# Kernel optimization log

Measured on AMD Instinct MI355X. Metric: run time of the kernel, lower is better.

The kernel has to match this reference:

```python
import jax, jax.numpy as jnp
import numpy as np

TEMPERATURE = 0.07
EPS = 1e-12  # matches F.normalize eps

def _l2norm(x, axis):
    n = jnp.sqrt(jnp.sum(x * x, axis=axis, keepdims=True))
    return x / jnp.maximum(n, EPS)

def setup_inputs() -> dict:
    key = jax.random.key(0)
    features = jax.random.normal(key, (512, 256), dtype=jnp.float32)
    return {"features": features}

def reference(features) -> jnp.ndarray:
    B = features.shape[0]
    f = _l2norm(features, axis=1)                      # [B, D]
    fi = f[:, None, :]                                 # broadcast over j
    fj = f[None, :, :]                                 # broadcast over i
    mutual = fi * fj                                   # [B, B, D]
    gate_i = fi * mutual
    gate_j = fj * mutual
    # torch broadcasting: + features adds f[j, k] along trailing dims
    feats_self_i = _l2norm(fi * gate_i + f, axis=2)
    feats_other_i = _l2norm(fi * gate_j + f, axis=2)
    feats_other_j = _l2norm(fj * gate_i + f, axis=2)
    # note: features_self_j is computed in the original but never used in any dot product

    raw_self_i = jnp.einsum('ik,ijk->ij', f, feats_self_i) / TEMPERATURE
    raw_self_j = jnp.einsum('ik,ijk->ij', f, feats_other_j) / TEMPERATURE  # (original uses other_j here)
    raw_other_i = jnp.einsum('ik,ijk->ij', f, feats_other_i) / TEMPERATURE
    raw_other_j = jnp.einsum('ik,ijk->ij', f, feats_other_j) / TEMPERATURE

    logits_mask = 1.0 - jnp.eye(B, dtype=f.dtype)      # zero out diagonal
    exp_sum = (jnp.exp(raw_self_i) + jnp.exp(raw_self_j)
               + jnp.exp(raw_other_i) + jnp.exp(raw_other_j)) * logits_mask
    vs_all = jnp.sum(exp_sum, axis=1, keepdims=True)   # [B, 1]

    log_prob = raw_self_i - jnp.log(vs_all)            # [B, B]
    mean_log_prob_pos = jnp.sum(log_prob, axis=1) / B
    loss = -jnp.mean(mean_log_prob_pos)
    return loss
```

## Files before the change

### kernel.cpp

```cpp
#include <hip/hip_runtime.h>
#include <math.h>

#define Bq 512
#define Dq 256

__device__ __forceinline__ float waveReduceSum(float v) {
    #pragma unroll
    for (int off = 32; off > 0; off >>= 1)
        v += __shfl_xor(v, off, 64);
    return v;
}

__global__ __launch_bounds__(256) void prep_kernel(
        const float* __restrict__ feat,
        float* __restrict__ fT, float* __restrict__ C1, float* __restrict__ C2,
        float* __restrict__ A1, float* __restrict__ A2) {
    int i = blockIdx.x;
    int k = threadIdx.x;
    float x = feat[i * Dq + k];
    float ss = waveReduceSum(x * x);
    __shared__ float wsum[4];
    int wid = threadIdx.x >> 6, lane = threadIdx.x & 63;
    if (lane == 0) wsum[wid] = ss;
    __syncthreads();
    float tot = wsum[0] + wsum[1] + wsum[2] + wsum[3];
    float n = fmaxf(sqrtf(tot), 1e-12f);
    float a = x / n;
    float a2 = a * a;
    float a3 = a2 * a;
    float c0 = 1.0f + a3;
    fT[k * Bq + i] = a;
    A1[i * Dq + k] = a;
    A2[i * Dq + k] = a2;
    C1[i * Dq + k] = a * c0;
    C2[i * Dq + k] = c0 * c0;
}

__global__ __launch_bounds__(512) void pair_kernel(
        const float* __restrict__ fT,
        const float* __restrict__ C1, const float* __restrict__ C2,
        const float* __restrict__ A1, const float* __restrict__ A2,
        float* __restrict__ Sv, float* __restrict__ Vv) {
    const int i = blockIdx.x;
    const int t = threadIdx.x;

    __shared__ __align__(16) float s_c1[Dq];
    __shared__ __align__(16) float s_c2[Dq];
    __shared__ __align__(16) float s_a1[Dq];
    __shared__ __align__(16) float s_a2[Dq];
    if (t < Dq) {
        s_c1[t] = C1[i * Dq + t];
        s_c2[t] = C2[i * Dq + t];
        s_a1[t] = A1[i * Dq + t];
        s_a2[t] = A2[i * Dq + t];
    }
    __syncthreads();

    float du = 0.f, nu = 0.f, dv = 0.f, nv = 0.f;
    const float* __restrict__ bp = fT + t;

    #pragma unroll 2
    for (int k0 = 0; k0 < Dq; k0 += 8) {
        float b[8];
        #pragma unroll
        for (int u = 0; u < 8; ++u) b[u] = bp[(k0 + u) * Bq];

        float4 q1a = *(const float4*)(s_c1 + k0), q1b = *(const float4*)(s_c1 + k0 + 4);
        float4 q2a = *(const float4*)(s_c2 + k0), q2b = *(const float4*)(s_c2 + k0 + 4);
        float4 q3a = *(const float4*)(s_a1 + k0), q3b = *(const float4*)(s_a1 + k0 + 4);
        float4 q4a = *(const float4*)(s_a2 + k0), q4b = *(const float4*)(s_a2 + k0 + 4);
        const float c1[8] = {q1a.x, q1a.y, q1a.z, q1a.w, q1b.x, q1b.y, q1b.z, q1b.w};
        const float c2[8] = {q2a.x, q2a.y, q2a.z, q2a.w, q2b.x, q2b.y, q2b.z, q2b.w};
        const float a1[8] = {q3a.x, q3a.y, q3a.z, q3a.w, q3b.x, q3b.y, q3b.z, q3b.w};
        const float a2[8] = {q4a.x, q4a.y, q4a.z, q4a.w, q4b.x, q4b.y, q4b.z, q4b.w};

        #pragma unroll
        for (int u = 0; u < 8; ++u) {
            float b1 = b[u];
            float bb = b1 * b1;
            float w  = fmaf(a2[u], b1, 1.0f);
            float wb = w * b1;
            du = fmaf(c1[u], b1, du);
            nu = fmaf(c2[u], bb, nu);
            dv = fmaf(a1[u], wb, dv);
            nv = fmaf(wb,    wb, nv);
        }
    }

    const float Tinv = 1.0f / 0.07f;
    float raw_s = du / fmaxf(sqrtf(nu), 1e-12f) * Tinv;
    float raw_o = dv / fmaxf(sqrtf(nv), 1e-12f) * Tinv;

    float sS = raw_s;
    float sV = (t == i) ? 0.f : (expf(raw_s) + 3.0f * expf(raw_o));

    sS = waveReduceSum(sS);
    sV = waveReduceSum(sV);
    __shared__ float redS[8], redV[8];
    int wid = t >> 6, lane = t & 63;
    if (lane == 0) { redS[wid] = sS; redV[wid] = sV; }
    __syncthreads();
    if (t == 0) {
        float S = 0.f, V = 0.f;
        #pragma unroll
        for (int w2 = 0; w2 < 8; ++w2) { S += redS[w2]; V += redV[w2]; }
        Sv[i] = S;
        Vv[i] = V;
    }
}

__global__ __launch_bounds__(512) void final_kernel(
        const float* __restrict__ Sv, const float* __restrict__ Vv,
        float* __restrict__ out) {
    int i = threadIdx.x;
    float t = Sv[i] * (1.0f / Bq) - logf(Vv[i]);
    t = waveReduceSum(t);
    __shared__ float red[8];
    int wid = i >> 6, lane = i & 63;
    if (lane == 0) red[wid] = t;
    __syncthreads();
    if (i == 0) {
        float s = 0.f;
        #pragma unroll
        for (int w = 0; w < 8; ++w) s += red[w];
        out[0] = -s / (float)Bq;
    }
}

extern "C" void kernel_launch(void* const* d_in, const int* in_sizes, int n_in,
                              void* d_out, int out_size, void* d_ws, size_t ws_size,
                              hipStream_t stream) {
    const float* feat = (const float*)d_in[0];
    float* ws = (float*)d_ws;
    float* fT = ws;
    float* C1 = fT + Bq * Dq;
    float* C2 = C1 + Bq * Dq;
    float* A1 = C2 + Bq * Dq;
    float* A2 = A1 + Bq * Dq;
    float* Sv = A2 + Bq * Dq;
    float* Vv = Sv + Bq;

    prep_kernel<<<Bq, Dq, 0, stream>>>(feat, fT, C1, C2, A1, A2);
    pair_kernel<<<Bq, 512, 0, stream>>>(fT, C1, C2, A1, A2, Sv, Vv);
    final_kernel<<<1, Bq, 0, stream>>>(Sv, Vv, (float*)d_out);
}
```

Measured before the change: 76.86 us.

## Compute per-row coefficients in pair kernel and fuse final reduction via last-block atomic

The prep kernel now writes only the transposed normalized features and per-row norms instead of four extra coefficient arrays. The pair kernel recomputes the coefficients from the raw features into shared memory. The separate final reduction kernel is removed: each block publishes its row term, and the last block to increment an atomic counter sums them. This cuts global writes and one kernel launch, at the cost of an atomic counter and a release/acquire handshake between blocks.

```diff
diff --git a/kernel.cpp b/kernel.cpp
--- a/kernel.cpp
+++ b/kernel.cpp
@@ -13,8 +13,8 @@
 
 __global__ __launch_bounds__(256) void prep_kernel(
         const float* __restrict__ feat,
-        float* __restrict__ fT, float* __restrict__ C1, float* __restrict__ C2,
-        float* __restrict__ A1, float* __restrict__ A2) {
+        float* __restrict__ fT, float* __restrict__ norms,
+        int* __restrict__ counter) {
     int i = blockIdx.x;
     int k = threadIdx.x;
     float x = feat[i * Dq + k];
@@ -25,22 +25,16 @@
     __syncthreads();
     float tot = wsum[0] + wsum[1] + wsum[2] + wsum[3];
     float n = fmaxf(sqrtf(tot), 1e-12f);
-    float a = x / n;
-    float a2 = a * a;
-    float a3 = a2 * a;
-    float c0 = 1.0f + a3;
-    fT[k * Bq + i] = a;
-    A1[i * Dq + k] = a;
-    A2[i * Dq + k] = a2;
-    C1[i * Dq + k] = a * c0;
-    C2[i * Dq + k] = c0 * c0;
+    fT[k * Bq + i] = x / n;
+    if (k == 0) norms[i] = n;
+    if (i == 0 && k == 0) *counter = 0;
 }
 
 __global__ __launch_bounds__(512) void pair_kernel(
-        const float* __restrict__ fT,
-        const float* __restrict__ C1, const float* __restrict__ C2,
-        const float* __restrict__ A1, const float* __restrict__ A2,
-        float* __restrict__ Sv, float* __restrict__ Vv) {
+        const float* __restrict__ feat,
+        const float* __restrict__ fT, const float* __restrict__ norms,
+        float* __restrict__ tws, int* __restrict__ counter,
+        float* __restrict__ out) {
     const int i = blockIdx.x;
     const int t = threadIdx.x;
 
@@ -49,10 +43,13 @@
     __shared__ __align__(16) float s_a1[Dq];
     __shared__ __align__(16) float s_a2[Dq];
     if (t < Dq) {
-        s_c1[t] = C1[i * Dq + t];
-        s_c2[t] = C2[i * Dq + t];
-        s_a1[t] = A1[i * Dq + t];
-        s_a2[t] = A2[i * Dq + t];
+        float a  = feat[i * Dq + t] / norms[i];
+        float a2 = a * a;
+        float c0 = 1.0f + a2 * a;
+        s_a1[t] = a;
+        s_a2[t] = a2;
+        s_c1[t] = a * c0;
+        s_c2[t] = c0 * c0;
     }
     __syncthreads();
 
@@ -100,30 +97,33 @@
     int wid = t >> 6, lane = t & 63;
     if (lane == 0) { redS[wid] = sS; redV[wid] = sV; }
     __syncthreads();
+
+    __shared__ int s_last;
     if (t == 0) {
         float S = 0.f, V = 0.f;
         #pragma unroll
         for (int w2 = 0; w2 < 8; ++w2) { S += redS[w2]; V += redV[w2]; }
-        Sv[i] = S;
-        Vv[i] = V;
+        float ti = S * (1.0f / Bq) - logf(V);
+        __hip_atomic_store(&tws[i], ti, __ATOMIC_RELEASE, __HIP_MEMORY_SCOPE_AGENT);
+        int old = __hip_atomic_fetch_add(counter, 1, __ATOMIC_ACQ_REL,
+                                         __HIP_MEMORY_SCOPE_AGENT);
+        s_last = (old == Bq - 1) ? 1 : 0;
     }
-}
+    __syncthreads();
 
-__global__ __launch_bounds__(512) void final_kernel(
-        const float* __restrict__ Sv, const float* __restrict__ Vv,
-        float* __restrict__ out) {
-    int i = threadIdx.x;
-    float t = Sv[i] * (1.0f / Bq) - logf(Vv[i]);
-    t = waveReduceSum(t);
-    __shared__ float red[8];
-    int wid = i >> 6, lane = i & 63;
-    if (lane == 0) red[wid] = t;
-    __syncthreads();
-    if (i == 0) {
-        float s = 0.f;
-        #pragma unroll
-        for (int w = 0; w < 8; ++w) s += red[w];
-        out[0] = -s / (float)Bq;
+    if (s_last) {
+        float v = __hip_atomic_load(&tws[t], __ATOMIC_RELAXED,
+                                    __HIP_MEMORY_SCOPE_AGENT);
+        float r = waveReduceSum(v);
+        __shared__ float red[8];
+        if (lane == 0) red[wid] = r;
+        __syncthreads();
+        if (t == 0) {
+            float s = 0.f;
+            #pragma unroll
+            for (int w = 0; w < 8; ++w) s += red[w];
+            out[0] = -s / (float)Bq;
+        }
     }
 }
 
@@ -132,15 +132,12 @@
                               hipStream_t stream) {
     const float* feat = (const float*)d_in[0];
     float* ws = (float*)d_ws;
-    float* fT = ws;
-    float* C1 = fT + Bq * Dq;
-    float* C2 = C1 + Bq * Dq;
-    float* A1 = C2 + Bq * Dq;
-    float* A2 = A1 + Bq * Dq;
-    float* Sv = A2 + Bq * Dq;
-    float* Vv = Sv + Bq;
+    float* fT    = ws;
+    float* norms = fT + Bq * Dq;
+    float* tws   = norms + Bq;
+    int*   counter = (int*)(tws + Bq);
 
-    prep_kernel<<<Bq, Dq, 0, stream>>>(feat, fT, C1, C2, A1, A2);
-    pair_kernel<<<Bq, 512, 0, stream>>>(fT, C1, C2, A1, A2, Sv, Vv);
-    final_kernel<<<1, Bq, 0, stream>>>(Sv, Vv, (float*)d_out);
+    prep_kernel<<<Bq, Dq, 0, stream>>>(feat, fT, norms, counter);
+    pair_kernel<<<Bq, 512, 0, stream>>>(feat, fT, norms, tws, counter,
+                                        (float*)d_out);
 }
```

New measurement: 86.37 us. 1.12x slower.

## Process two rows per block and compute per-row coefficients on the fly

Applied to the files above, without the earlier changes.

Each pair_kernel block now handles two rows i, so each column load from fT feeds two sets of accumulators. This halves global traffic on fT and the grid size. The prep kernel no longer writes the four coefficient arrays and emits only fT plus per-row norms, and pair_kernel rebuilds the coefficients in shared memory. This trades more registers per thread and fewer blocks (256 of them) for less memory traffic, which may reduce occupancy or under-fill the GPU.

```diff
diff --git a/kernel.cpp b/kernel.cpp
--- a/kernel.cpp
+++ b/kernel.cpp
@@ -13,8 +13,7 @@
 
 __global__ __launch_bounds__(256) void prep_kernel(
         const float* __restrict__ feat,
-        float* __restrict__ fT, float* __restrict__ C1, float* __restrict__ C2,
-        float* __restrict__ A1, float* __restrict__ A2) {
+        float* __restrict__ fT, float* __restrict__ norms) {
     int i = blockIdx.x;
     int k = threadIdx.x;
     float x = feat[i * Dq + k];
@@ -25,87 +24,114 @@
     __syncthreads();
     float tot = wsum[0] + wsum[1] + wsum[2] + wsum[3];
     float n = fmaxf(sqrtf(tot), 1e-12f);
-    float a = x / n;
-    float a2 = a * a;
-    float a3 = a2 * a;
-    float c0 = 1.0f + a3;
-    fT[k * Bq + i] = a;
-    A1[i * Dq + k] = a;
-    A2[i * Dq + k] = a2;
-    C1[i * Dq + k] = a * c0;
-    C2[i * Dq + k] = c0 * c0;
+    fT[k * Bq + i] = x / n;
+    if (k == 0) norms[i] = n;
 }
 
 __global__ __launch_bounds__(512) void pair_kernel(
-        const float* __restrict__ fT,
-        const float* __restrict__ C1, const float* __restrict__ C2,
-        const float* __restrict__ A1, const float* __restrict__ A2,
+        const float* __restrict__ feat,
+        const float* __restrict__ fT, const float* __restrict__ norms,
         float* __restrict__ Sv, float* __restrict__ Vv) {
-    const int i = blockIdx.x;
+    const int i0 = blockIdx.x * 2;
     const int t = threadIdx.x;
 
-    __shared__ __align__(16) float s_c1[Dq];
-    __shared__ __align__(16) float s_c2[Dq];
-    __shared__ __align__(16) float s_a1[Dq];
-    __shared__ __align__(16) float s_a2[Dq];
-    if (t < Dq) {
-        s_c1[t] = C1[i * Dq + t];
-        s_c2[t] = C2[i * Dq + t];
-        s_a1[t] = A1[i * Dq + t];
-        s_a2[t] = A2[i * Dq + t];
+    __shared__ __align__(16) float s_c1[2][Dq];
+    __shared__ __align__(16) float s_c2[2][Dq];
+    __shared__ __align__(16) float s_a1[2][Dq];
+    __shared__ __align__(16) float s_a2[2][Dq];
+    {
+        int ci = t >> 8;
+        int ck = t & 255;
+        float a  = feat[(i0 + ci) * Dq + ck] / norms[i0 + ci];
+        float a2 = a * a;
+        float c0 = 1.0f + a2 * a;
+        s_a1[ci][ck] = a;
+        s_a2[ci][ck] = a2;
+        s_c1[ci][ck] = a * c0;
+        s_c2[ci][ck] = c0 * c0;
     }
     __syncthreads();
 
-    float du = 0.f, nu = 0.f, dv = 0.f, nv = 0.f;
+    float du0 = 0.f, nu0 = 0.f, dv0 = 0.f, nv0 = 0.f;
+    float du1 = 0.f, nu1 = 0.f, dv1 = 0.f, nv1 = 0.f;
     const float* __restrict__ bp = fT + t;
 
-    #pragma unroll 2
     for (int k0 = 0; k0 < Dq; k0 += 8) {
         float b[8];
         #pragma unroll
         for (int u = 0; u < 8; ++u) b[u] = bp[(k0 + u) * Bq];
 
-        float4 q1a = *(const float4*)(s_c1 + k0), q1b = *(const float4*)(s_c1 + k0 + 4);
-        float4 q2a = *(const float4*)(s_c2 + k0), q2b = *(const float4*)(s_c2 + k0 + 4);
-        float4 q3a = *(const float4*)(s_a1 + k0), q3b = *(const float4*)(s_a1 + k0 + 4);
-        float4 q4a = *(const float4*)(s_a2 + k0), q4b = *(const float4*)(s_a2 + k0 + 4);
-        const float c1[8] = {q1a.x, q1a.y, q1a.z, q1a.w, q1b.x, q1b.y, q1b.z, q1b.w};
-        const float c2[8] = {q2a.x, q2a.y, q2a.z, q2a.w, q2b.x, q2b.y, q2b.z, q2b.w};
-        const float a1[8] = {q3a.x, q3a.y, q3a.z, q3a.w, q3b.x, q3b.y, q3b.z, q3b.w};
-        const float a2[8] = {q4a.x, q4a.y, q4a.z, q4a.w, q4b.x, q4b.y, q4b.z, q4b.w};
+        float4 p0a = *(const float4*)(&s_c1[0][k0]), p0b = *(const float4*)(&s_c1[0][k0 + 4]);
+        float4 p1a = *(const float4*)(&s_c2[0][k0]), p1b = *(const float4*)(&s_c2[0][k0 + 4]);
+        float4 p2a = *(const float4*)(&s_a1[0][k0]), p2b = *(const float4*)(&s_a1[0][k0 + 4]);
+        float4 p3a = *(const float4*)(&s_a2[0][k0]), p3b = *(const float4*)(&s_a2[0][k0 + 4]);
+        float4 q0a = *(const float4*)(&s_c1[1][k0]), q0b = *(const float4*)(&s_c1[1][k0 + 4]);
+        float4 q1a = *(const float4*)(&s_c2[1][k0]), q1b = *(const float4*)(&s_c2[1][k0 + 4]);
+        float4 q2a = *(const float4*)(&s_a1[1][k0]), q2b = *(const float4*)(&s_a1[1][k0 + 4]);
+        float4 q3a = *(const float4*)(&s_a2[1][k0]), q3b = *(const float4*)(&s_a2[1][k0 + 4]);
+        const float c1_0[8] = {p0a.x, p0a.y, p0a.z, p0a.w, p0b.x, p0b.y, p0b.z, p0b.w};
+        const float c2_0[8] = {p1a.x, p1a.y, p1a.z, p1a.w, p1b.x, p1b.y, p1b.z, p1b.w};
+        const float a1_0[8] = {p2a.x, p2a.y, p2a.z, p2a.w, p2b.x, p2b.y, p2b.z, p2b.w};
+        const float a2_0[8] = {p3a.x, p3a.y, p3a.z, p3a.w, p3b.x, p3b.y, p3b.z, p3b.w};
+        const float c1_1[8] = {q0a.x, q0a.y, q0a.z, q0a.w, q0b.x, q0b.y, q0b.z, q0b.w};
+        const float c2_1[8] = {q1a.x, q1a.y, q1a.z, q1a.w, q1b.x, q1b.y, q1b.z, q1b.w};
+        const float a1_1[8] = {q2a.x, q2a.y, q2a.z, q2a.w, q2b.x, q2b.y, q2b.z, q2b.w};
+        const float a2_1[8] = {q3a.x, q3a.y, q3a.z, q3a.w, q3b.x, q3b.y, q3b.z, q3b.w};
 
         #pragma unroll
         for (int u = 0; u < 8; ++u) {
             float b1 = b[u];
             float bb = b1 * b1;
-            float w  = fmaf(a2[u], b1, 1.0f);
-            float wb = w * b1;
-            du = fmaf(c1[u], b1, du);
-            nu = fmaf(c2[u], bb, nu);
-            dv = fmaf(a1[u], wb, dv);
-            nv = fmaf(wb,    wb, nv);
+            {
+                float w  = fmaf(a2_0[u], b1, 1.0f);
+                float wb = w * b1;
+                du0 = fmaf(c1_0[u], b1, du0);
+                nu0 = fmaf(c2_0[u], bb, nu0);
+                dv0 = fmaf(a1_0[u], wb, dv0);
+                nv0 = fmaf(wb,      wb, nv0);
+            }
+            {
+                float w  = fmaf(a2_1[u], b1, 1.0f);
+                float wb = w * b1;
+                du1 = fmaf(c1_1[u], b1, du1);
+                nu1 = fmaf(c2_1[u], bb, nu1);
+                dv1 = fmaf(a1_1[u], wb, dv1);
+                nv1 = fmaf(wb,      wb, nv1);
+            }
         }
     }
 
     const float Tinv = 1.0f / 0.07f;
-    float raw_s = du / fmaxf(sqrtf(nu), 1e-12f) * Tinv;
-    float raw_o = dv / fmaxf(sqrtf(nv), 1e-12f) * Tinv;
+    float raw_s0 = du0 / fmaxf(sqrtf(nu0), 1e-12f) * Tinv;
+    float raw_o0 = dv0 / fmaxf(sqrtf(nv0), 1e-12f) * Tinv;
+    float raw_s1 = du1 / fmaxf(sqrtf(nu1), 1e-12f) * Tinv;
+    float raw_o1 = dv1 / fmaxf(sqrtf(nv1), 1e-12f) * Tinv;
 
-    float sS = raw_s;
-    float sV = (t == i) ? 0.f : (expf(raw_s) + 3.0f * expf(raw_o));
+    float sS0 = raw_s0;
+    float sV0 = (t == i0)     ? 0.f : (expf(raw_s0) + 3.0f * expf(raw_o0));
+    float sS1 = raw_s1;
+    float sV1 = (t == i0 + 1) ? 0.f : (expf(raw_s1) + 3.0f * expf(raw_o1));
 
-    sS = waveReduceSum(sS);
-    sV = waveReduceSum(sV);
-    __shared__ float redS[8], redV[8];
+    sS0 = waveReduceSum(sS0);
+    sV0 = waveReduceSum(sV0);
+    sS1 = waveReduceSum(sS1);
+    sV1 = waveReduceSum(sV1);
+    __shared__ float redS[2][8], redV[2][8];
     int wid = t >> 6, lane = t & 63;
-    if (lane == 0) { redS[wid] = sS; redV[wid] = sV; }
+    if (lane == 0) {
+        redS[0][wid] = sS0; redV[0][wid] = sV0;
+        redS[1][wid] = sS1; redV[1][wid] = sV1;
+    }
     __syncthreads();
     if (t == 0) {
-        float S = 0.f, V = 0.f;
+        float S0 = 0.f, V0 = 0.f, S1 = 0.f, V1 = 0.f;
         #pragma unroll
-        for (int w2 = 0; w2 < 8; ++w2) { S += redS[w2]; V += redV[w2]; }
-        Sv[i] = S;
-        Vv[i] = V;
+        for (int w2 = 0; w2 < 8; ++w2) {
+            S0 += redS[0][w2]; V0 += redV[0][w2];
+            S1 += redS[1][w2]; V1 += redV[1][w2];
+        }
+        Sv[i0] = S0;     Vv[i0] = V0;
+        Sv[i0 + 1] = S1; Vv[i0 + 1] = V1;
     }
 }
 
@@ -132,15 +158,12 @@
                               hipStream_t stream) {
     const float* feat = (const float*)d_in[0];
     float* ws = (float*)d_ws;
-    float* fT = ws;
-    float* C1 = fT + Bq * Dq;
-    float* C2 = C1 + Bq * Dq;
-    float* A1 = C2 + Bq * Dq;
-    float* A2 = A1 + Bq * Dq;
-    float* Sv = A2 + Bq * Dq;
-    float* Vv = Sv + Bq;
+    float* fT    = ws;
+    float* norms = fT + Bq * Dq;
+    float* Sv    = norms + Bq;
+    float* Vv    = Sv + Bq;
 
-    prep_kernel<<<Bq, Dq, 0, stream>>>(feat, fT, C1, C2, A1, A2);
-    pair_kernel<<<Bq, 512, 0, stream>>>(fT, C1, C2, A1, A2, Sv, Vv);
+    prep_kernel<<<Bq, Dq, 0, stream>>>(feat, fT, norms);
+    pair_kernel<<<Bq / 2, 512, 0, stream>>>(feat, fT, norms, Sv, Vv);
     final_kernel<<<1, Bq, 0, stream>>>(Sv, Vv, (float*)d_out);
 }
```

Result: slower. 83.12 us (+8.1%).

## Recast pairwise reductions as split-fp16 MFMA matrix products with atomic row sums

Applied to the files above, without the earlier changes.

Rewrites the per-pair reductions as matrix products on the MFMA units. Operands are stored as fp16 hi/lo pairs so the dominant terms keep close to fp32 accuracy, and the norm is expanded algebraically into 1 + 2·a²·b³ + a⁴b⁴ terms, with a scaled fp16 term for the quartic part. The grid becomes 32x32 output tiles per block, and row sums are accumulated with atomics instead of one block per row. The aim is to replace scalar FMA throughput with matrix-core throughput. The cost is precision loss on the single-fp16 cubic and quartic terms and reliance on atomic accumulation.

```diff
diff --git a/kernel.cpp b/kernel.cpp
--- a/kernel.cpp
+++ b/kernel.cpp
@@ -3,6 +3,10 @@
 
 #define Bq 512
 #define Dq 256
+#define MS (Bq * Dq)
+
+typedef _Float16 f16x8 __attribute__((ext_vector_type(8)));
+typedef float f32x4 __attribute__((ext_vector_type(4)));
 
 __device__ __forceinline__ float waveReduceSum(float v) {
     #pragma unroll
@@ -11,101 +15,131 @@
     return v;
 }
 
+__device__ __forceinline__ void split16(float x, _Float16* h, _Float16* l) {
+    _Float16 hh = (_Float16)x;
+    *h = hh;
+    *l = (_Float16)(x - (float)hh);
+}
+
 __global__ __launch_bounds__(256) void prep_kernel(
-        const float* __restrict__ feat,
-        float* __restrict__ fT, float* __restrict__ C1, float* __restrict__ C2,
-        float* __restrict__ A1, float* __restrict__ A2) {
-    int i = blockIdx.x;
+        const float* __restrict__ feat, _Float16* __restrict__ M,
+        float* __restrict__ S, float* __restrict__ V) {
+    int r = blockIdx.x;
     int k = threadIdx.x;
-    float x = feat[i * Dq + k];
+    float x = feat[r * Dq + k];
     float ss = waveReduceSum(x * x);
     __shared__ float wsum[4];
-    int wid = threadIdx.x >> 6, lane = threadIdx.x & 63;
+    int wid = k >> 6, lane = k & 63;
     if (lane == 0) wsum[wid] = ss;
     __syncthreads();
-    float tot = wsum[0] + wsum[1] + wsum[2] + wsum[3];
-    float n = fmaxf(sqrtf(tot), 1e-12f);
+    float n = fmaxf(sqrtf(wsum[0] + wsum[1] + wsum[2] + wsum[3]), 1e-12f);
     float a = x / n;
-    float a2 = a * a;
-    float a3 = a2 * a;
-    float c0 = 1.0f + a3;
-    fT[k * Bq + i] = a;
-    A1[i * Dq + k] = a;
-    A2[i * Dq + k] = a2;
-    C1[i * Dq + k] = a * c0;
-    C2[i * Dq + k] = c0 * c0;
+    float a2 = a * a, a3 = a2 * a, a4 = a2 * a2;
+    float c1 = a * (1.0f + a3);
+    float c2 = (1.0f + a3) * (1.0f + a3);
+    int o = r * Dq + k;
+    _Float16 h, l;
+    split16(c1, &h, &l); M[0 * MS + o] = h; M[1 * MS + o] = l;
+    split16(c2, &h, &l); M[2 * MS + o] = h; M[3 * MS + o] = l;
+    split16(a,  &h, &l); M[4 * MS + o] = h; M[5 * MS + o] = l;
+    split16(a2, &h, &l); M[6 * MS + o] = h; M[7 * MS + o] = l;
+    M[8 * MS + o] = (_Float16)a3;
+    M[9 * MS + o] = (_Float16)(a4 * 64.0f);
+    if (r == 0) {
+        S[k] = 0.f; S[k + 256] = 0.f;
+        V[k] = 0.f; V[k + 256] = 0.f;
+    }
 }
 
-__global__ __launch_bounds__(512) void pair_kernel(
-        const float* __restrict__ fT,
-        const float* __restrict__ C1, const float* __restrict__ C2,
-        const float* __restrict__ A1, const float* __restrict__ A2,
-        float* __restrict__ Sv, float* __restrict__ Vv) {
-    const int i = blockIdx.x;
+__global__ __launch_bounds__(256) void pairmm_kernel(
+        const _Float16* __restrict__ M,
+        float* __restrict__ S, float* __restrict__ V) {
     const int t = threadIdx.x;
+    const int w = t >> 6, lane = t & 63;
+    const int lr = lane & 15, lg = lane >> 4;
+    const int bx = blockIdx.x;
+    const int it = (bx >> 4) * 32 + (w >> 1) * 16;
+    const int jt = (bx & 15) * 32 + (w & 1) * 16;
+    const int offi = (it + lr) * Dq + lg * 8;
+    const int offj = (jt + lr) * Dq + lg * 8;
 
-    __shared__ __align__(16) float s_c1[Dq];
-    __shared__ __align__(16) float s_c2[Dq];
-    __shared__ __align__(16) float s_a1[Dq];
-    __shared__ __align__(16) float s_a2[Dq];
-    if (t < Dq) {
-        s_c1[t] = C1[i * Dq + t];
-        s_c2[t] = C2[i * Dq + t];
-        s_a1[t] = A1[i * Dq + t];
-        s_a2[t] = A2[i * Dq + t];
-    }
-    __syncthreads();
+    const _Float16* __restrict__ C1h = M;
+    const _Float16* __restrict__ C1l = M + 1 * MS;
+    const _Float16* __restrict__ C2h = M + 2 * MS;
+    const _Float16* __restrict__ C2l = M + 3 * MS;
+    const _Float16* __restrict__ Ah  = M + 4 * MS;
+    const _Float16* __restrict__ Al  = M + 5 * MS;
+    const _Float16* __restrict__ A2h = M + 6 * MS;
+    const _Float16* __restrict__ A2l = M + 7 * MS;
+    const _Float16* __restrict__ A3h = M + 8 * MS;
+    const _Float16* __restrict__ A4h = M + 9 * MS;
 
-    float du = 0.f, nu = 0.f, dv = 0.f, nv = 0.f;
-    const float* __restrict__ bp = fT + t;
+    f32x4 du = {0.f, 0.f, 0.f, 0.f};
+    f32x4 nu = {0.f, 0.f, 0.f, 0.f};
+    f32x4 dv = {0.f, 0.f, 0.f, 0.f};
+    f32x4 n3 = {0.f, 0.f, 0.f, 0.f};
+    f32x4 n4 = {0.f, 0.f, 0.f, 0.f};
 
     #pragma unroll 2
-    for (int k0 = 0; k0 < Dq; k0 += 8) {
-        float b[8];
-        #pragma unroll
-        for (int u = 0; u < 8; ++u) b[u] = bp[(k0 + u) * Bq];
+    for (int kk = 0; kk < Dq; kk += 32) {
+        int oi = offi + kk, oj = offj + kk;
+        f16x8 c1h = *(const f16x8*)(C1h + oi);
+        f16x8 c1l = *(const f16x8*)(C1l + oi);
+        f16x8 c2h = *(const f16x8*)(C2h + oi);
+        f16x8 c2l = *(const f16x8*)(C2l + oi);
+        f16x8 ahi = *(const f16x8*)(Ah  + oi);
+        f16x8 ali = *(const f16x8*)(Al  + oi);
+        f16x8 a2i = *(const f16x8*)(A2h + oi);
+        f16x8 a3i = *(const f16x8*)(A3h + oi);
+        f16x8 a4i = *(const f16x8*)(A4h + oi);
+        f16x8 ahj = *(const f16x8*)(Ah  + oj);
+        f16x8 alj = *(const f16x8*)(Al  + oj);
+        f16x8 a2j = *(const f16x8*)(A2h + oj);
+        f16x8 a2lj = *(const f16x8*)(A2l + oj);
+        f16x8 a3j = *(const f16x8*)(A3h + oj);
+        f16x8 a4j = *(const f16x8*)(A4h + oj);
 
-        float4 q1a = *(const float4*)(s_c1 + k0), q1b = *(const float4*)(s_c1 + k0 + 4);
-        float4 q2a = *(const float4*)(s_c2 + k0), q2b = *(const float4*)(s_c2 + k0 + 4);
-        float4 q3a = *(const float4*)(s_a1 + k0), q3b = *(const float4*)(s_a1 + k0 + 4);
-        float4 q4a = *(const float4*)(s_a2 + k0), q4b = *(const float4*)(s_a2 + k0 + 4);
-        const float c1[8] = {q1a.x, q1a.y, q1a.z, q1a.w, q1b.x, q1b.y, q1b.z, q1b.w};
-        const float c2[8] = {q2a.x, q2a.y, q2a.z, q2a.w, q2b.x, q2b.y, q2b.z, q2b.w};
-        const float a1[8] = {q3a.x, q3a.y, q3a.z, q3a.w, q3b.x, q3b.y, q3b.z, q3b.w};
-        const float a2[8] = {q4a.x, q4a.y, q4a.z, q4a.w, q4b.x, q4b.y, q4b.z, q4b.w};
-
-        #pragma unroll
-        for (int u = 0; u < 8; ++u) {
-            float b1 = b[u];
-            float bb = b1 * b1;
-            float w  = fmaf(a2[u], b1, 1.0f);
-            float wb = w * b1;
-            du = fmaf(c1[u], b1, du);
-            nu = fmaf(c2[u], bb, nu);
-            dv = fmaf(a1[u], wb, dv);
-            nv = fmaf(wb,    wb, nv);
-        }
+        du = __builtin_amdgcn_mfma_f32_16x16x32_f16(c1h, ahj,  du, 0, 0, 0);
+        du = __builtin_amdgcn_mfma_f32_16x16x32_f16(c1h, alj,  du, 0, 0, 0);
+        du = __builtin_amdgcn_mfma_f32_16x16x32_f16(c1l, ahj,  du, 0, 0, 0);
+        nu = __builtin_amdgcn_mfma_f32_16x16x32_f16(c2h, a2j,  nu, 0, 0, 0);
+        nu = __builtin_amdgcn_mfma_f32_16x16x32_f16(c2h, a2lj, nu, 0, 0, 0);
+        nu = __builtin_amdgcn_mfma_f32_16x16x32_f16(c2l, a2j,  nu, 0, 0, 0);
+        dv = __builtin_amdgcn_mfma_f32_16x16x32_f16(ahi, ahj,  dv, 0, 0, 0);
+        dv = __builtin_amdgcn_mfma_f32_16x16x32_f16(ahi, alj,  dv, 0, 0, 0);
+        dv = __builtin_amdgcn_mfma_f32_16x16x32_f16(ali, ahj,  dv, 0, 0, 0);
+        dv = __builtin_amdgcn_mfma_f32_16x16x32_f16(a3i, a2j,  dv, 0, 0, 0);
+        n3 = __builtin_amdgcn_mfma_f32_16x16x32_f16(a2i, a3j,  n3, 0, 0, 0);
+        n4 = __builtin_amdgcn_mfma_f32_16x16x32_f16(a4i, a4j,  n4, 0, 0, 0);
     }
 
     const float Tinv = 1.0f / 0.07f;
-    float raw_s = du / fmaxf(sqrtf(nu), 1e-12f) * Tinv;
-    float raw_o = dv / fmaxf(sqrtf(nv), 1e-12f) * Tinv;
-
-    float sS = raw_s;
-    float sV = (t == i) ? 0.f : (expf(raw_s) + 3.0f * expf(raw_o));
-
-    sS = waveReduceSum(sS);
-    sV = waveReduceSum(sV);
-    __shared__ float redS[8], redV[8];
-    int wid = t >> 6, lane = t & 63;
-    if (lane == 0) { redS[wid] = sS; redV[wid] = sV; }
-    __syncthreads();
-    if (t == 0) {
-        float S = 0.f, V = 0.f;
+    float sS[4], sV[4];
+    #pragma unroll
+    for (int r = 0; r < 4; ++r) {
+        float nuv = fmaxf(nu[r], 0.f);
+        float nvv = fmaxf(1.0f + 2.0f * n3[r] + n4[r] * (1.0f / 4096.0f), 0.f);
+        float raw_s = du[r] / fmaxf(sqrtf(nuv), 1e-12f) * Tinv;
+        float raw_o = dv[r] / fmaxf(sqrtf(nvv), 1e-12f) * Tinv;
+        int gi = it + lg * 4 + r;
+        int gj = jt + lr;
+        sS[r] = raw_s;
+        sV[r] = (gi == gj) ? 0.f : (expf(raw_s) + 3.0f * expf(raw_o));
+    }
+    #pragma unroll
+    for (int r = 0; r < 4; ++r) {
         #pragma unroll
-        for (int w2 = 0; w2 < 8; ++w2) { S += redS[w2]; V += redV[w2]; }
-        Sv[i] = S;
-        Vv[i] = V;
+        for (int m = 1; m < 16; m <<= 1) {
+            sS[r] += __shfl_xor(sS[r], m, 64);
+            sV[r] += __shfl_xor(sV[r], m, 64);
+        }
+    }
+    if (lr == 0) {
+        #pragma unroll
+        for (int r = 0; r < 4; ++r) {
+            atomicAdd(&S[it + lg * 4 + r], sS[r]);
+            atomicAdd(&V[it + lg * 4 + r], sV[r]);
+        }
     }
 }
 
@@ -131,16 +165,11 @@
                               void* d_out, int out_size, void* d_ws, size_t ws_size,
                               hipStream_t stream) {
     const float* feat = (const float*)d_in[0];
-    float* ws = (float*)d_ws;
-    float* fT = ws;
-    float* C1 = fT + Bq * Dq;
-    float* C2 = C1 + Bq * Dq;
-    float* A1 = C2 + Bq * Dq;
-    float* A2 = A1 + Bq * Dq;
-    float* Sv = A2 + Bq * Dq;
-    float* Vv = Sv + Bq;
+    _Float16* M = (_Float16*)d_ws;
+    float* S = (float*)((char*)d_ws + (size_t)10 * MS * sizeof(_Float16));
+    float* V = S + Bq;
 
-    prep_kernel<<<Bq, Dq, 0, stream>>>(feat, fT, C1, C2, A1, A2);
-    pair_kernel<<<Bq, 512, 0, stream>>>(fT, C1, C2, A1, A2, Sv, Vv);
-    final_kernel<<<1, Bq, 0, stream>>>(Sv, Vv, (float*)d_out);
+    prep_kernel<<<Bq, Dq, 0, stream>>>(feat, M, S, V);
+    pairmm_kernel<<<256, 256, 0, stream>>>(M, S, V);
+    final_kernel<<<1, Bq, 0, stream>>>(S, V, (float*)d_out);
 }
```

After: 76.26 us. Within noise of the previous version (-0.8%).
